# Performance work log

Hardware: AMD Instinct MI355X
Metric: run time of the kernel (lower is better)

## Reference

```python
import jax, jax.numpy as jnp
import numpy as np

B, S, D, H, DFF = 2, 4096, 768, 12, 3072
DH = D // H
EPS = 1e-6


def layer_norm(x, gamma, beta):
    # torch.std is unbiased (ddof=1); normalizer is (sigma + eps), NOT sqrt(var+eps)
    mu = jnp.mean(x, axis=-1, keepdims=True)
    sigma = jnp.sqrt(jnp.var(x, axis=-1, keepdims=True, ddof=1))
    return gamma * (x - mu) / (sigma + EPS) + beta


def setup_inputs() -> dict:
    key = jax.random.key(0)
    ks = jax.random.split(key, 12)
    sc = 1.0 / np.sqrt(D)
    inp = {
        "x": jax.random.normal(ks[0], (B, S, D), dtype=jnp.float32),
        "mask": jnp.ones((B, S, S), dtype=jnp.float32),  # multiplicative mask
        "wq": jax.random.normal(ks[1], (D, D), dtype=jnp.float32) * sc,
        "bq": jnp.zeros((D,), dtype=jnp.float32),
        "wk": jax.random.normal(ks[2], (D, D), dtype=jnp.float32) * sc,
        "bk": jnp.zeros((D,), dtype=jnp.float32),
        "wv": jax.random.normal(ks[3], (D, D), dtype=jnp.float32) * sc,
        "bv": jnp.zeros((D,), dtype=jnp.float32),
        "wo": jax.random.normal(ks[4], (D, D), dtype=jnp.float32) * sc,
        "bo": jnp.zeros((D,), dtype=jnp.float32),
        "w1": jax.random.normal(ks[5], (D, DFF), dtype=jnp.float32) * sc,
        "b1": jnp.zeros((DFF,), dtype=jnp.float32),
        "w2": jax.random.normal(ks[6], (DFF, D), dtype=jnp.float32) * (1.0 / np.sqrt(DFF)),
        "b2": jnp.zeros((D,), dtype=jnp.float32),
        "gamma1": jnp.ones((D,), dtype=jnp.float32),
        "beta1": jnp.zeros((D,), dtype=jnp.float32),
        "gamma2": jnp.ones((D,), dtype=jnp.float32),
        "beta2": jnp.zeros((D,), dtype=jnp.float32),
    }
    return inp


def reference(x, mask, wq, bq, wk, bk, wv, bv, wo, bo, w1, b1, w2, b2,
              gamma1, beta1, gamma2, beta2):
    # Pre-LN encoder layer (is_pre_layer_norm=True); dropout is identity (eval).
    l1 = layer_norm(x, gamma1, beta1)                      # [B,S,D]

    # --- multi-head self-attention ---
    q = (l1 @ wq + bq).reshape(B, S, H, DH).transpose(0, 2, 1, 3)  # [B,H,S,DH]
    k = (l1 @ wk + bk).reshape(B, S, H, DH).transpose(0, 2, 1, 3)
    v = (l1 @ wv + bv).reshape(B, S, H, DH).transpose(0, 2, 1, 3)
    scores = jnp.einsum("bhqd,bhkd->bhqk", q, k) / jnp.sqrt(jnp.float32(DH))
    scores = scores * mask[:, None, :, :]                  # multiplicative mask, pre-softmax
    attn = jax.nn.softmax(scores, axis=-1)                 # [B,H,S,S]
    ctx = jnp.einsum("bhqk,bhkd->bhqd", attn, v)           # [B,H,S,DH]
    ctx = ctx.transpose(0, 2, 1, 3).reshape(B, S, D)       # [B,S,D]
    a = ctx  # NOTE: original forward never applies out_linear in attention()... it does in forward
    a = ctx
    # MultiHeadAttention.forward returns the merged heads WITHOUT out_linear applied?
    # Re-check: forward() reshapes and returns `output` without out_linear in given code.
    x1 = x + a                                             # residual

    l2 = layer_norm(x1, gamma2, beta2)
    h = jax.nn.relu(l2 @ w1 + b1) @ w2 + b2                # FFN
    return h + x1
```

## Files before the change

kernel.cpp:

```cpp
#include <hip/hip_runtime.h>
#include <cstdint>
#include <cstddef>

#define BB   2
#define SEQ  4096
#define DD   768
#define HH   12
#define DHH  64
#define DFFN 3072
#define NTOK (BB*SEQ)

using bf16x8 = __attribute__((ext_vector_type(8))) __bf16;
using f32x4  = __attribute__((ext_vector_type(4))) float;
typedef unsigned int u32;

#define QK_SCALE 0.18033688011112042f

__device__ __forceinline__ float fast_exp2(float x) {
    return __builtin_amdgcn_exp2f(x);
}

__device__ __forceinline__ unsigned short f2bf(float f) {
    unsigned u = __float_as_uint(f);
    u = u + 0x7FFFu + ((u >> 16) & 1u);
    return (unsigned short)(u >> 16);
}
__device__ __forceinline__ unsigned short f2bf_trunc(float f) {
    return (unsigned short)(__float_as_uint(f) >> 16);
}

__device__ __forceinline__ bf16x8 ld_bf8(const unsigned short* p) {
    return *(const bf16x8*)p;
}

__device__ __forceinline__ void gl_lds16(const unsigned short* g, unsigned short* l) {
    __builtin_amdgcn_global_load_lds(
        (const __attribute__((address_space(1))) u32*)(uintptr_t)(const void*)g,
        (__attribute__((address_space(3))) u32*)(uintptr_t)(void*)l,
        16, 0, 0);
}

template <int N>
__device__ __forceinline__ float dpp_ror(float x) {
    return __int_as_float(__builtin_amdgcn_update_dpp(
        0, __float_as_int(x), 0x120 | N, 0xf, 0xf, false));
}
__device__ __forceinline__ float rowmax16(float x) {
    x = fmaxf(x, dpp_ror<1>(x));
    x = fmaxf(x, dpp_ror<2>(x));
    x = fmaxf(x, dpp_ror<4>(x));
    x = fmaxf(x, dpp_ror<8>(x));
    return x;
}
__device__ __forceinline__ float rowsum16(float x) {
    x += dpp_ror<1>(x);
    x += dpp_ror<2>(x);
    x += dpp_ror<4>(x);
    x += dpp_ror<8>(x);
    return x;
}

__global__ __launch_bounds__(256) void transpose_f32_to_bf16(
    const float* __restrict__ src, unsigned short* __restrict__ dst, int R, int C, float scale)
{
    __shared__ float tile[32][33];
    const int c0 = blockIdx.x * 32, r0 = blockIdx.y * 32;
    const int tx = threadIdx.x, ty = threadIdx.y;
#pragma unroll
    for (int i = 0; i < 32; i += 8)
        tile[ty + i][tx] = src[(size_t)(r0 + ty + i) * C + c0 + tx];
    __syncthreads();
#pragma unroll
    for (int i = 0; i < 32; i += 8)
        dst[(size_t)(c0 + ty + i) * R + r0 + tx] = f2bf(scale * tile[tx][ty + i]);
}

__global__ void concat_bias(const float* __restrict__ bq, const float* __restrict__ bk,
                            const float* __restrict__ bv, float* __restrict__ bqkv)
{
    int i = blockIdx.x * 256 + threadIdx.x;
    if (i < 3 * DD)
        bqkv[i] = (i < DD) ? bq[i] * QK_SCALE : (i < 2 * DD ? bk[i - DD] : bv[i - 2 * DD]);
}

__global__ __launch_bounds__(256) void mask_check(const float* __restrict__ mask, int* __restrict__ flag)
{
    const size_t n = (size_t)BB * SEQ * SEQ;
    const size_t stride = (size_t)gridDim.x * 1024;
    int bad = 0;
    for (size_t i = ((size_t)blockIdx.x * 256 + threadIdx.x) * 4; i < n; i += stride) {
        float4 v = *(const float4*)&mask[i];
        bad |= (v.x != 1.f) | (v.y != 1.f) | (v.z != 1.f) | (v.w != 1.f);
    }
    if (bad) atomicOr(flag, 1);
}

__global__ __launch_bounds__(256) void ln_fused(
    const float* __restrict__ x, const float* __restrict__ add,
    const float* __restrict__ gamma, const float* __restrict__ beta,
    unsigned short* __restrict__ out_ln, float* __restrict__ x1out)
{
    const int row = blockIdx.x, t = threadIdx.x;
    const size_t base = (size_t)row * DD;
    float v[3], s = 0.f, sq = 0.f;
#pragma unroll
    for (int p = 0; p < 3; ++p) {
        int idx = t + p * 256;
        float val = x[base + idx];
        if (add) val += add[base + idx];
        v[p] = val; s += val; sq += val * val;
    }
#pragma unroll
    for (int off = 1; off < 64; off <<= 1) {
        s  += __shfl_xor(s,  off);
        sq += __shfl_xor(sq, off);
    }
    __shared__ float red[8];
    const int wave = t >> 6;
    if ((t & 63) == 0) { red[wave] = s; red[4 + wave] = sq; }
    __syncthreads();
    s  = red[0] + red[1] + red[2] + red[3];
    sq = red[4] + red[5] + red[6] + red[7];
    const float mu   = s * (1.f / 768.f);
    const float var  = fmaxf((sq - 768.f * mu * mu) * (1.f / 767.f), 0.f);
    const float rstd = 1.f / (sqrtf(var) + 1e-6f);
#pragma unroll
    for (int p = 0; p < 3; ++p) {
        int idx = t + p * 256;
        if (x1out) x1out[base + idx] = v[p];
        out_ln[base + idx] = f2bf(gamma[idx] * (v[p] - mu) * rstd + beta[idx]);
    }
}

__global__ __launch_bounds__(256) void gemm_bf16(
    const unsigned short* __restrict__ A, const unsigned short* __restrict__ Bt,
    const float* __restrict__ bias, const float* __restrict__ resid,
    unsigned short* __restrict__ outB, float* __restrict__ outF,
    int M, int N, int K, int relu)
{
    __shared__ __align__(16) unsigned short As[128][64];
    __shared__ __align__(16) unsigned short Bs[128][64];
    const int tid = threadIdx.x;
    const int lane = tid & 63, wave = tid >> 6;
    const int quad = lane >> 4, l16 = lane & 15;
    const int wm = wave >> 1, wn = wave & 1;
    const int m0 = blockIdx.y * 128, n0 = blockIdx.x * 128;

    const f32x4 fzero = {0.f, 0.f, 0.f, 0.f};
    f32x4 acc[4][4];
#pragma unroll
    for (int i = 0; i < 4; ++i)
#pragma unroll
        for (int j = 0; j < 4; ++j) acc[i][j] = fzero;

    const int r  = tid >> 3;
    const int cg = tid & 7;

    for (int k0 = 0; k0 < K; k0 += 64) {
#pragma unroll
        for (int rr = 0; rr < 4; ++rr) {
            const int row = r + rr * 32;
            const int gc8 = (cg ^ (row & 7)) * 8;
            gl_lds16(&A [(size_t)(m0 + row) * K + k0 + gc8], &As[row][cg * 8]);
            gl_lds16(&Bt[(size_t)(n0 + row) * K + k0 + gc8], &Bs[row][cg * 8]);
        }
        __syncthreads();
#pragma unroll
        for (int ks = 0; ks < 2; ++ks) {
            bf16x8 af[4], bfv[4];
#pragma unroll
            for (int i = 0; i < 4; ++i) {
                const int row = wm * 64 + i * 16 + l16;
                af[i] = ld_bf8(&As[row][((ks * 4 + quad) ^ (row & 7)) * 8]);
            }
#pragma unroll
            for (int j = 0; j < 4; ++j) {
                const int row = wn * 64 + j * 16 + l16;
                bfv[j] = ld_bf8(&Bs[row][((ks * 4 + quad) ^ (row & 7)) * 8]);
            }
#pragma unroll
            for (int i = 0; i < 4; ++i)
#pragma unroll
                for (int j = 0; j < 4; ++j)
                    acc[i][j] = __builtin_amdgcn_mfma_f32_16x16x32_bf16(af[i], bfv[j], acc[i][j], 0, 0, 0);
        }
        __syncthreads();
    }
#pragma unroll
    for (int i = 0; i < 4; ++i)
#pragma unroll
        for (int j = 0; j < 4; ++j)
#pragma unroll
            for (int rr = 0; rr < 4; ++rr) {
                const int gm = m0 + wm * 64 + i * 16 + quad * 4 + rr;
                const int gn = n0 + wn * 64 + j * 16 + l16;
                float v = acc[i][j][rr] + bias[gn];
                if (relu) v = fmaxf(v, 0.f);
                if (resid) v += resid[(size_t)gm * N + gn];
                if (outF) outF[(size_t)gm * N + gn] = v;
                if (outB) outB[(size_t)gm * N + gn] = f2bf(v);
            }
}

__global__ __launch_bounds__(256) void vt_extract(
    const unsigned short* __restrict__ qkv, unsigned short* __restrict__ vtg)
{
    __shared__ unsigned short tile[64][72];
    const int bh = blockIdx.x, b = bh / HH, h = bh % HH;
    const int s0 = blockIdx.y * 64;
    const int tid = threadIdx.x;
#pragma unroll
    for (int p = 0; p < 2; ++p) {
        int idx = tid + p * 256;
        int r = idx >> 3, ch8 = (idx & 7) * 8;
        *(uint4*)&tile[r][ch8] =
            *(const uint4*)&qkv[(size_t)(b * SEQ + s0 + r) * 2304 + 1536 + h * 64 + ch8];
    }
    __syncthreads();
#pragma unroll
    for (int p = 0; p < 2; ++p) {
        int idx = tid + p * 256;
        int d = idx >> 3, sc = (idx & 7) * 8;
        unsigned short tmp[8];
#pragma unroll
        for (int j = 0; j < 8; ++j) tmp[j] = tile[sc + j][d];
        *(uint4*)&vtg[((size_t)bh * 64 + d) * SEQ + s0 + sc] = *(uint4*)tmp;
    }
}

__global__ __launch_bounds__(256, 2) void flash_attn5(
    const unsigned short* __restrict__ qkv, const unsigned short* __restrict__ vtg,
    const float* __restrict__ mask, const int* __restrict__ maskflag,
    float* __restrict__ ctx)
{
    __shared__ __align__(16) unsigned short Ks[128][72];
    __shared__ __align__(16) unsigned short Vt[64][136];
    __shared__ __align__(16) unsigned short Ps[4][2][16][136];
    const int tid = threadIdx.x;
    const int lane = tid & 63, wave = tid >> 6;
    const int quad = lane >> 4, l16 = lane & 15;
    const int bh = blockIdx.y, b = bh / HH, h = bh % HH;
    const int qbase = blockIdx.x * 128 + wave * 32;
    const int use_mask = *maskflag;

    bf16x8 qf[2][2];
#pragma unroll
    for (int mt = 0; mt < 2; ++mt) {
        const size_t qrow = (size_t)(b * SEQ + qbase + mt * 16 + l16) * 2304 + h * 64;
        qf[mt][0] = ld_bf8(&qkv[qrow + quad * 8]);
        qf[mt][1] = ld_bf8(&qkv[qrow + 32 + quad * 8]);
    }
    const f32x4 fzero = {0.f, 0.f, 0.f, 0.f};
    float l_run[2][4];
    f32x4 o[2][4];
#pragma unroll
    for (int mt = 0; mt < 2; ++mt)
#pragma unroll
        for (int r = 0; r < 4; ++r) { l_run[mt][r] = 0.f; o[mt][r] = fzero; }

    const float* mbase = mask + (size_t)b * SEQ * SEQ;
    const unsigned short* kgbase = qkv + (size_t)b * SEQ * 2304 + 768 + h * 64;
    const unsigned short* vgbase = vtg + (size_t)bh * 64 * SEQ;

    if (!use_mask) {
        float lsum[2][4];
#pragma unroll
        for (int mt = 0; mt < 2; ++mt)
#pragma unroll
            for (int r = 0; r < 4; ++r) lsum[mt][r] = 0.f;

        for (int k0 = 0; k0 < SEQ; k0 += 128) {
            __syncthreads();
#pragma unroll
            for (int p = 0; p < 4; ++p) {
                int idx = tid + p * 256;
                int row = idx >> 3, ch8 = (idx & 7) * 8;
                *(uint4*)&Ks[row][ch8] = *(const uint4*)&kgbase[(size_t)(k0 + row) * 2304 + ch8];
            }
#pragma unroll
            for (int p = 0; p < 4; ++p) {
                int idx = tid + p * 256;
                int d = idx >> 4, ch8 = (idx & 15) * 8;
                *(uint4*)&Vt[d][ch8] = *(const uint4*)&vgbase[(size_t)d * SEQ + k0 + ch8];
            }
            __syncthreads();

            f32x4 st[2][8];
#pragma unroll
            for (int j = 0; j < 8; ++j) {
                bf16x8 kf0 = ld_bf8(&Ks[j * 16 + l16][quad * 8]);
                bf16x8 kf1 = ld_bf8(&Ks[j * 16 + l16][32 + quad * 8]);
                st[0][j] = __builtin_amdgcn_mfma_f32_16x16x32_bf16(qf[0][0], kf0, fzero, 0, 0, 0);
                st[0][j] = __builtin_amdgcn_mfma_f32_16x16x32_bf16(qf[0][1], kf1, st[0][j], 0, 0, 0);
                st[1][j] = __builtin_amdgcn_mfma_f32_16x16x32_bf16(qf[1][0], kf0, fzero, 0, 0, 0);
                st[1][j] = __builtin_amdgcn_mfma_f32_16x16x32_bf16(qf[1][1], kf1, st[1][j], 0, 0, 0);
            }
#pragma unroll
            for (int mt = 0; mt < 2; ++mt) {
#pragma unroll
                for (int r = 0; r < 4; ++r) {
                    float acc = 0.f;
#pragma unroll
                    for (int j = 0; j < 8; ++j) {
                        float p = fast_exp2(st[mt][j][r]);
                        st[mt][j][r] = p;
                        acc += p;
                    }
                    lsum[mt][r] += acc;
                }
#pragma unroll
                for (int j = 0; j < 8; ++j)
#pragma unroll
                    for (int r = 0; r < 4; ++r)
                        Ps[wave][mt][quad * 4 + r][j * 16 + l16] = f2bf_trunc(st[mt][j][r]);
            }
#pragma unroll
            for (int kk = 0; kk < 4; ++kk) {
                bf16x8 pf0 = ld_bf8(&Ps[wave][0][l16][kk * 32 + quad * 8]);
                bf16x8 pf1 = ld_bf8(&Ps[wave][1][l16][kk * 32 + quad * 8]);
#pragma unroll
                for (int t = 0; t < 4; ++t) {
                    bf16x8 vf = ld_bf8(&Vt[t * 16 + l16][kk * 32 + quad * 8]);
                    o[0][t] = __builtin_amdgcn_mfma_f32_16x16x32_bf16(pf0, vf, o[0][t], 0, 0, 0);
                    o[1][t] = __builtin_amdgcn_mfma_f32_16x16x32_bf16(pf1, vf, o[1][t], 0, 0, 0);
                }
            }
        }
#pragma unroll
        for (int mt = 0; mt < 2; ++mt)
#pragma unroll
            for (int r = 0; r < 4; ++r) l_run[mt][r] = rowsum16(lsum[mt][r]);
    } else {
        float m_run[2][4];
#pragma unroll
        for (int mt = 0; mt < 2; ++mt)
#pragma unroll
            for (int r = 0; r < 4; ++r) m_run[mt][r] = -1e30f;

        for (int k0 = 0; k0 < SEQ; k0 += 128) {
            __syncthreads();
#pragma unroll
            for (int p = 0; p < 4; ++p) {
                int idx = tid + p * 256;
                int row = idx >> 3, ch8 = (idx & 7) * 8;
                *(uint4*)&Ks[row][ch8] = *(const uint4*)&kgbase[(size_t)(k0 + row) * 2304 + ch8];
            }
#pragma unroll
            for (int p = 0; p < 4; ++p) {
                int idx = tid + p * 256;
                int d = idx >> 4, ch8 = (idx & 15) * 8;
                *(uint4*)&Vt[d][ch8] = *(const uint4*)&vgbase[(size_t)d * SEQ + k0 + ch8];
            }
            __syncthreads();

            f32x4 st[2][8];
#pragma unroll
            for (int j = 0; j < 8; ++j) {
                bf16x8 kf0 = ld_bf8(&Ks[j * 16 + l16][quad * 8]);
                bf16x8 kf1 = ld_bf8(&Ks[j * 16 + l16][32 + quad * 8]);
                st[0][j] = __builtin_amdgcn_mfma_f32_16x16x32_bf16(qf[0][0], kf0, fzero, 0, 0, 0);
                st[0][j] = __builtin_amdgcn_mfma_f32_16x16x32_bf16(qf[0][1], kf1, st[0][j], 0, 0, 0);
                st[1][j] = __builtin_amdgcn_mfma_f32_16x16x32_bf16(qf[1][0], kf0, fzero, 0, 0, 0);
                st[1][j] = __builtin_amdgcn_mfma_f32_16x16x32_bf16(qf[1][1], kf1, st[1][j], 0, 0, 0);
            }
#pragma unroll
            for (int mt = 0; mt < 2; ++mt) {
                const int qr = qbase + mt * 16 + quad * 4;
#pragma unroll
                for (int r = 0; r < 4; ++r) {
                    const float* mrow = &mbase[(size_t)(qr + r) * SEQ + k0 + l16];
#pragma unroll
                    for (int j = 0; j < 8; ++j)
                        st[mt][j][r] *= mrow[j * 16];
                }
            }
#pragma unroll
            for (int mt = 0; mt < 2; ++mt) {
                float alpha[4];
#pragma unroll
                for (int r = 0; r < 4; ++r) {
                    float mx = st[mt][0][r];
#pragma unroll
                    for (int j = 1; j < 8; ++j) mx = fmaxf(mx, st[mt][j][r]);
                    mx = rowmax16(mx);
                    const float mnew = fmaxf(m_run[mt][r], mx);
                    alpha[r] = fast_exp2(m_run[mt][r] - mnew);
                    float ssum = 0.f;
#pragma unroll
                    for (int j = 0; j < 8; ++j) {
                        st[mt][j][r] = fast_exp2(st[mt][j][r] - mnew);
                        ssum += st[mt][j][r];
                    }
                    ssum = rowsum16(ssum);
                    l_run[mt][r] = l_run[mt][r] * alpha[r] + ssum;
                    m_run[mt][r] = mnew;
                }
#pragma unroll
                for (int t = 0; t < 4; ++t)
#pragma unroll
                    for (int r = 0; r < 4; ++r) o[mt][t][r] *= alpha[r];
#pragma unroll
                for (int j = 0; j < 8; ++j)
#pragma unroll
                    for (int r = 0; r < 4; ++r)
                        Ps[wave][mt][quad * 4 + r][j * 16 + l16] = f2bf_trunc(st[mt][j][r]);
            }
#pragma unroll
            for (int kk = 0; kk < 4; ++kk) {
                bf16x8 pf0 = ld_bf8(&Ps[wave][0][l16][kk * 32 + quad * 8]);
                bf16x8 pf1 = ld_bf8(&Ps[wave][1][l16][kk * 32 + quad * 8]);
#pragma unroll
                for (int t = 0; t < 4; ++t) {
                    bf16x8 vf = ld_bf8(&Vt[t * 16 + l16][kk * 32 + quad * 8]);
                    o[0][t] = __builtin_amdgcn_mfma_f32_16x16x32_bf16(pf0, vf, o[0][t], 0, 0, 0);
                    o[1][t] = __builtin_amdgcn_mfma_f32_16x16x32_bf16(pf1, vf, o[1][t], 0, 0, 0);
                }
            }
        }
    }

#pragma unroll
    for (int mt = 0; mt < 2; ++mt)
#pragma unroll
        for (int t = 0; t < 4; ++t)
#pragma unroll
            for (int r = 0; r < 4; ++r) {
                const int row = qbase + mt * 16 + quad * 4 + r;
                ctx[(size_t)(b * SEQ + row) * DD + h * 64 + t * 16 + l16] =
                    o[mt][t][r] / l_run[mt][r];
            }
}

extern "C" void kernel_launch(void* const* d_in, const int* in_sizes, int n_in,
                              void* d_out, int out_size, void* d_ws, size_t ws_size,
                              hipStream_t stream)
{
    (void)in_sizes; (void)n_in; (void)out_size; (void)ws_size;
    const float* x      = (const float*)d_in[0];
    const float* mask   = (const float*)d_in[1];
    const float* wq     = (const float*)d_in[2];
    const float* bq     = (const float*)d_in[3];
    const float* wk     = (const float*)d_in[4];
    const float* bk     = (const float*)d_in[5];
    const float* wv     = (const float*)d_in[6];
    const float* bv     = (const float*)d_in[7];
    const float* w1     = (const float*)d_in[10];
    const float* b1     = (const float*)d_in[11];
    const float* w2     = (const float*)d_in[12];
    const float* b2     = (const float*)d_in[13];
    const float* gamma1 = (const float*)d_in[14];
    const float* beta1  = (const float*)d_in[15];
    const float* gamma2 = (const float*)d_in[16];
    const float* beta2  = (const float*)d_in[17];
    float* out = (float*)d_out;

    char* ws = (char*)d_ws;
    size_t off = 0;
    auto take = [&](size_t bytes) -> char* {
        char* p = ws + off;
        off = (off + bytes + 255) & ~(size_t)255;
        return p;
    };
    unsigned short* wqkvT = (unsigned short*)take((size_t)2304 * 768 * 2);
    unsigned short* w1T   = (unsigned short*)take((size_t)3072 * 768 * 2);
    unsigned short* w2T   = (unsigned short*)take((size_t)768 * 3072 * 2);
    float*          bqkv  = (float*)take(2304 * 4);
    int*            mflag = (int*)take(256);
    unsigned short* l12   = (unsigned short*)take((size_t)NTOK * DD * 2);
    unsigned short* qkv   = (unsigned short*)take((size_t)NTOK * 2304 * 2);
    float*          x1    = (float*)take((size_t)NTOK * DD * 4);
    char*           big   = take((size_t)NTOK * DFFN * 2);
    float*          ctx   = (float*)big;
    unsigned short* vtg   = (unsigned short*)(big + (size_t)NTOK * DD * 4);
    unsigned short* hb    = (unsigned short*)big;

    (void)hipMemsetAsync(mflag, 0, 4, stream);
    mask_check<<<2048, 256, 0, stream>>>(mask, mflag);

    transpose_f32_to_bf16<<<dim3(24, 24), dim3(32, 8), 0, stream>>>(wq, wqkvT,                 768, 768, QK_SCALE);
    transpose_f32_to_bf16<<<dim3(24, 24), dim3(32, 8), 0, stream>>>(wk, wqkvT + 768 * 768,     768, 768, 1.0f);
    transpose_f32_to_bf16<<<dim3(24, 24), dim3(32, 8), 0, stream>>>(wv, wqkvT + 2 * 768 * 768, 768, 768, 1.0f);
    transpose_f32_to_bf16<<<dim3(96, 24), dim3(32, 8), 0, stream>>>(w1, w1T,                   768, 3072, 1.0f);
    transpose_f32_to_bf16<<<dim3(24, 96), dim3(32, 8), 0, stream>>>(w2, w2T,                   3072, 768, 1.0f);
    concat_bias<<<9, 256, 0, stream>>>(bq, bk, bv, bqkv);

    ln_fused<<<NTOK, 256, 0, stream>>>(x, nullptr, gamma1, beta1, l12, nullptr);
    gemm_bf16<<<dim3(2304 / 128, NTOK / 128), 256, 0, stream>>>(
        l12, wqkvT, bqkv, nullptr, qkv, nullptr, NTOK, 2304, 768, 0);
    vt_extract<<<dim3(BB * HH, SEQ / 64), 256, 0, stream>>>(qkv, vtg);
    flash_attn5<<<dim3(SEQ / 128, BB * HH), 256, 0, stream>>>(qkv, vtg, mask, mflag, ctx);
    ln_fused<<<NTOK, 256, 0, stream>>>(x, ctx, gamma2, beta2, l12, x1);
    gemm_bf16<<<dim3(3072 / 128, NTOK / 128), 256, 0, stream>>>(
        l12, w1T, b1, nullptr, hb, nullptr, NTOK, 3072, 768, 1);
    gemm_bf16<<<dim3(768 / 128, NTOK / 128), 256, 0, stream>>>(
        hb, w2T, b2, x1, nullptr, out, NTOK, 768, 3072, 0);
}
```

Baseline: 675.8 us.

## Load K and V fragments directly from global memory in flash attention

```diff
diff --git a/kernel.cpp b/kernel.cpp
--- a/kernel.cpp
+++ b/kernel.cpp
@@ -228,13 +228,11 @@
     }
 }
 
-__global__ __launch_bounds__(256, 2) void flash_attn5(
+__global__ __launch_bounds__(256, 3) void flash_attn7(
     const unsigned short* __restrict__ qkv, const unsigned short* __restrict__ vtg,
     const float* __restrict__ mask, const int* __restrict__ maskflag,
     float* __restrict__ ctx)
 {
-    __shared__ __align__(16) unsigned short Ks[128][72];
-    __shared__ __align__(16) unsigned short Vt[64][136];
     __shared__ __align__(16) unsigned short Ps[4][2][16][136];
     const int tid = threadIdx.x;
     const int lane = tid & 63, wave = tid >> 6;
@@ -270,26 +268,12 @@
             for (int r = 0; r < 4; ++r) lsum[mt][r] = 0.f;
 
         for (int k0 = 0; k0 < SEQ; k0 += 128) {
-            __syncthreads();
-#pragma unroll
-            for (int p = 0; p < 4; ++p) {
-                int idx = tid + p * 256;
-                int row = idx >> 3, ch8 = (idx & 7) * 8;
-                *(uint4*)&Ks[row][ch8] = *(const uint4*)&kgbase[(size_t)(k0 + row) * 2304 + ch8];
-            }
-#pragma unroll
-            for (int p = 0; p < 4; ++p) {
-                int idx = tid + p * 256;
-                int d = idx >> 4, ch8 = (idx & 15) * 8;
-                *(uint4*)&Vt[d][ch8] = *(const uint4*)&vgbase[(size_t)d * SEQ + k0 + ch8];
-            }
-            __syncthreads();
-
             f32x4 st[2][8];
 #pragma unroll
             for (int j = 0; j < 8; ++j) {
-                bf16x8 kf0 = ld_bf8(&Ks[j * 16 + l16][quad * 8]);
-                bf16x8 kf1 = ld_bf8(&Ks[j * 16 + l16][32 + quad * 8]);
+                const size_t krow = (size_t)(k0 + j * 16 + l16) * 2304;
+                bf16x8 kf0 = ld_bf8(&kgbase[krow + quad * 8]);
+                bf16x8 kf1 = ld_bf8(&kgbase[krow + 32 + quad * 8]);
                 st[0][j] = __builtin_amdgcn_mfma_f32_16x16x32_bf16(qf[0][0], kf0, fzero, 0, 0, 0);
                 st[0][j] = __builtin_amdgcn_mfma_f32_16x16x32_bf16(qf[0][1], kf1, st[0][j], 0, 0, 0);
                 st[1][j] = __builtin_amdgcn_mfma_f32_16x16x32_bf16(qf[1][0], kf0, fzero, 0, 0, 0);
@@ -320,7 +304,7 @@
                 bf16x8 pf1 = ld_bf8(&Ps[wave][1][l16][kk * 32 + quad * 8]);
 #pragma unroll
                 for (int t = 0; t < 4; ++t) {
-                    bf16x8 vf = ld_bf8(&Vt[t * 16 + l16][kk * 32 + quad * 8]);
+                    bf16x8 vf = ld_bf8(&vgbase[(size_t)(t * 16 + l16) * SEQ + k0 + kk * 32 + quad * 8]);
                     o[0][t] = __builtin_amdgcn_mfma_f32_16x16x32_bf16(pf0, vf, o[0][t], 0, 0, 0);
                     o[1][t] = __builtin_amdgcn_mfma_f32_16x16x32_bf16(pf1, vf, o[1][t], 0, 0, 0);
                 }
@@ -338,26 +322,12 @@
             for (int r = 0; r < 4; ++r) m_run[mt][r] = -1e30f;
 
         for (int k0 = 0; k0 < SEQ; k0 += 128) {
-            __syncthreads();
-#pragma unroll
-            for (int p = 0; p < 4; ++p) {
-                int idx = tid + p * 256;
-                int row = idx >> 3, ch8 = (idx & 7) * 8;
-                *(uint4*)&Ks[row][ch8] = *(const uint4*)&kgbase[(size_t)(k0 + row) * 2304 + ch8];
-            }
-#pragma unroll
-            for (int p = 0; p < 4; ++p) {
-                int idx = tid + p * 256;
-                int d = idx >> 4, ch8 = (idx & 15) * 8;
-                *(uint4*)&Vt[d][ch8] = *(const uint4*)&vgbase[(size_t)d * SEQ + k0 + ch8];
-            }
-            __syncthreads();
-
             f32x4 st[2][8];
 #pragma unroll
             for (int j = 0; j < 8; ++j) {
-                bf16x8 kf0 = ld_bf8(&Ks[j * 16 + l16][quad * 8]);
-                bf16x8 kf1 = ld_bf8(&Ks[j * 16 + l16][32 + quad * 8]);
+                const size_t krow = (size_t)(k0 + j * 16 + l16) * 2304;
+                bf16x8 kf0 = ld_bf8(&kgbase[krow + quad * 8]);
+                bf16x8 kf1 = ld_bf8(&kgbase[krow + 32 + quad * 8]);
                 st[0][j] = __builtin_amdgcn_mfma_f32_16x16x32_bf16(qf[0][0], kf0, fzero, 0, 0, 0);
                 st[0][j] = __builtin_amdgcn_mfma_f32_16x16x32_bf16(qf[0][1], kf1, st[0][j], 0, 0, 0);
                 st[1][j] = __builtin_amdgcn_mfma_f32_16x16x32_bf16(qf[1][0], kf0, fzero, 0, 0, 0);
@@ -411,7 +381,7 @@
                 bf16x8 pf1 = ld_bf8(&Ps[wave][1][l16][kk * 32 + quad * 8]);
 #pragma unroll
                 for (int t = 0; t < 4; ++t) {
-                    bf16x8 vf = ld_bf8(&Vt[t * 16 + l16][kk * 32 + quad * 8]);
+                    bf16x8 vf = ld_bf8(&vgbase[(size_t)(t * 16 + l16) * SEQ + k0 + kk * 32 + quad * 8]);
                     o[0][t] = __builtin_amdgcn_mfma_f32_16x16x32_bf16(pf0, vf, o[0][t], 0, 0, 0);
                     o[1][t] = __builtin_amdgcn_mfma_f32_16x16x32_bf16(pf1, vf, o[1][t], 0, 0, 0);
                 }
@@ -488,7 +458,7 @@
     gemm_bf16<<<dim3(2304 / 128, NTOK / 128), 256, 0, stream>>>(
         l12, wqkvT, bqkv, nullptr, qkv, nullptr, NTOK, 2304, 768, 0);
     vt_extract<<<dim3(BB * HH, SEQ / 64), 256, 0, stream>>>(qkv, vtg);
-    flash_attn5<<<dim3(SEQ / 128, BB * HH), 256, 0, stream>>>(qkv, vtg, mask, mflag, ctx);
+    flash_attn7<<<dim3(SEQ / 128, BB * HH), 256, 0, stream>>>(qkv, vtg, mask, mflag, ctx);
     ln_fused<<<NTOK, 256, 0, stream>>>(x, ctx, gamma2, beta2, l12, x1);
     gemm_bf16<<<dim3(3072 / 128, NTOK / 128), 256, 0, stream>>>(
         l12, w1T, b1, nullptr, hb, nullptr, NTOK, 3072, 768, 1);
```

After: 857.7 us. +26.9%, slower.
